# Performance work log

Hardware: AMD Instinct MI355X
Metric: run time of the kernel (lower is better)

## Reference

```python
import jax, jax.numpy as jnp
import numpy as np

N, T, D, H = 128, 64, 1024, 1024
DA = 4  # spatial dim of feature map


def setup_inputs() -> dict:
    key = jax.random.key(0)
    k1, k2, k3, k4, k5 = jax.random.split(key, 5)
    x = jax.random.normal(k1, (N, T, D), dtype=jnp.float32)
    A = jax.random.normal(k2, (N, H, DA, DA), dtype=jnp.float32)
    Wx = jax.random.normal(k3, (D, 4 * H), dtype=jnp.float32) / np.sqrt(D)
    Wh = jax.random.normal(k4, (H, 4 * H), dtype=jnp.float32) / np.sqrt(H)
    Wattn = jax.random.normal(k5, (H, 4 * H), dtype=jnp.float32) / np.sqrt(H)
    b = jnp.zeros((4 * H,), dtype=jnp.float32)
    return {"x": x, "A": A, "Wx": Wx, "Wh": Wh, "Wattn": Wattn, "b": b}


def _dot_product_attention(prev_h, A_flat):
    # prev_h: (N, H), A_flat: (N, H, L) with L = DA*DA
    scores = jnp.einsum('nh,nhl->nl', prev_h, A_flat) / jnp.sqrt(jnp.float32(H))
    w = jax.nn.softmax(scores, axis=-1)              # (N, L)
    attn = jnp.einsum('nhl,nl->nh', A_flat, w)       # (N, H)
    return attn


def reference(x, A, Wx, Wh, Wattn, b):
    A_flat = A.reshape(A.shape[0], A.shape[1], -1)   # (N, H, L)
    h0 = A.mean(axis=(2, 3))                          # (N, H)
    c0 = h0
    x_t = jnp.swapaxes(x, 0, 1)                       # (T, N, D)

    def step(carry, xt):
        h, c = carry
        attn = _dot_product_attention(h, A_flat)
        a = xt @ Wx + h @ Wh + attn @ Wattn + b       # (N, 4H)
        i, f, o, g = jnp.split(a, 4, axis=1)
        i = jax.nn.sigmoid(i)
        f = jax.nn.sigmoid(f)
        o = jax.nn.sigmoid(o)
        g = jnp.tanh(g)
        c_next = f * c + i * g
        h_next = o * jnp.tanh(c_next)
        return (h_next, c_next), h_next

    _, hn = jax.lax.scan(step, (h0, c0), x_t)         # hn: (T, N, H)
    return jnp.swapaxes(hn, 0, 1)                      # (N, T, H)
```

## Files before the change

kernel.cpp:

```cpp
#include <hip/hip_runtime.h>
#include <stdint.h>
#include <math.h>

typedef __attribute__((ext_vector_type(8))) short short8;
typedef __attribute__((ext_vector_type(4))) short short4v;
typedef __attribute__((ext_vector_type(4))) float f32x4;

__device__ __forceinline__ short f2bf(float f){
  union { float f; uint32_t u; } x; x.f = f;
  uint32_t r = x.u + 0x7fffu + ((x.u >> 16) & 1u);
  return (short)(r >> 16);
}
__device__ __forceinline__ float bf2f(short s){
  union { uint32_t u; float f; } x; x.u = ((uint32_t)(uint16_t)s) << 16;
  return x.f;
}

__device__ __forceinline__ unsigned ld_llc_u32(const void* p){
  return __hip_atomic_load((const unsigned*)p, __ATOMIC_RELAXED, __HIP_MEMORY_SCOPE_AGENT);
}
__device__ __forceinline__ void st_llc_u32(void* p, unsigned v){
  __hip_atomic_store((unsigned*)p, v, __ATOMIC_RELAXED, __HIP_MEMORY_SCOPE_AGENT);
}


__global__ __launch_bounds__(256) void k_wt(const float* __restrict__ Wx,
                                            const float* __restrict__ Wh,
                                            const float* __restrict__ Wattn,
                                            short* __restrict__ W3T){
  __shared__ float tile[64][65];
  int bk = blockIdx.x % 48, bj = blockIdx.x / 48;
  int tx = threadIdx.x & 63, ty = threadIdx.x >> 6;
  int k0 = bk * 64, j0 = bj * 64;
  #pragma unroll
  for (int i = 0; i < 16; ++i){
    int kk = ty * 16 + i;
    int k = k0 + kk;
    const float* src = (k < 1024) ? (Wx + (size_t)k * 4096)
                     : (k < 2048) ? (Wh + (size_t)(k - 1024) * 4096)
                                  : (Wattn + (size_t)(k - 2048) * 4096);
    tile[kk][tx] = src[j0 + tx];
  }
  __syncthreads();
  #pragma unroll
  for (int i = 0; i < 16; ++i){
    int jj = ty * 16 + i;
    W3T[(size_t)(j0 + jj) * 3072 + k0 + tx] = f2bf(tile[tx][jj]);
  }
}

__global__ __launch_bounds__(256) void k_cast(const float* __restrict__ in,
                                              short* __restrict__ out, int n4){
  int i = blockIdx.x * 256 + threadIdx.x;
  if (i >= n4) return;
  float4 v = ((const float4*)in)[i];
  short4v o; o[0] = f2bf(v.x); o[1] = f2bf(v.y); o[2] = f2bf(v.z); o[3] = f2bf(v.w);
  *(short4v*)(out + (size_t)i * 4) = o;
}

__global__ __launch_bounds__(256) void k_castA(const float* __restrict__ A,
                                               short* __restrict__ Abf,
                                               short* __restrict__ Atr){
  const int n = blockIdx.x;
  const int tid = threadIdx.x;
  __shared__ short tile[256][17];
  for (int it = 0; it < 4; ++it){
    int h = it * 256 + tid;
    const float* src = A + ((size_t)n * 1024 + h) * 16;
    short o[16];
    #pragma unroll
    for (int l = 0; l < 16; ++l) o[l] = f2bf(src[l]);
    short8 p0, p1;
    #pragma unroll
    for (int l = 0; l < 8; ++l){ p0[l] = o[l]; p1[l] = o[8 + l]; }
    short8* dst = (short8*)(Abf + ((size_t)n * 1024 + h) * 16);
    dst[0] = p0; dst[1] = p1;
    #pragma unroll
    for (int l = 0; l < 16; ++l) tile[tid][l] = o[l];
    __syncthreads();
    {
      int l = tid >> 4, hc = (tid & 15) * 16;
      short tmp[16];
      #pragma unroll
      for (int k = 0; k < 16; ++k) tmp[k] = tile[hc + k][l];
      short8 q0, q1;
      #pragma unroll
      for (int k = 0; k < 8; ++k){ q0[k] = tmp[k]; q1[k] = tmp[8 + k]; }
      short8* d2 = (short8*)(Atr + (size_t)n * 16384 + l * 1024 + it * 256 + hc);
      d2[0] = q0; d2[1] = q1;
    }
    __syncthreads();
  }
}

__global__ __launch_bounds__(256) void k_init(const float* __restrict__ A,
                                              float* __restrict__ c,
                                              short* __restrict__ hb0,
                                              unsigned* __restrict__ flags){
  int idx = blockIdx.x * 256 + threadIdx.x;
  if (idx < 8192) flags[idx] = 0u;
  const float* p = A + (size_t)idx * 16;
  float s = 0.f;
  #pragma unroll
  for (int l = 0; l < 16; ++l) s += p[l];
  s *= (1.f / 16.f);
  c[idx] = s;
  hb0[idx] = f2bf(s);
}

typedef const __attribute__((address_space(1))) uint32_t* gas1_t;
typedef __attribute__((address_space(3))) uint32_t* las3_t;

__global__ __launch_bounds__(256) void k_xwx(const short* __restrict__ xbf,
                                             const short* __restrict__ W3T,
                                             short* __restrict__ xwx){
  __shared__ short ldsA[128 * 64];
  __shared__ short ldsB[128 * 64];
  const int tid  = threadIdx.x;
  const int lane = tid & 63;
  const int wave = tid >> 6;
  const int orig = blockIdx.x;
  const int wg = (orig & 7) * 256 + (orig >> 3);
  const int n_t = wg >> 6;
  const int m_t = wg & 63;
  const int m0 = m_t * 128;
  const int n0 = n_t * 128;
  const int ra = lane & 15;
  const int q  = lane >> 4;

  f32x4 acc[4][4];
  #pragma unroll
  for (int mf = 0; mf < 4; ++mf)
    #pragma unroll
    for (int jf = 0; jf < 4; ++jf) acc[mf][jf] = f32x4{0.f,0.f,0.f,0.f};

  const int wm = wave >> 1;
  const int wn = wave & 1;

  for (int kt = 0; kt < 16; ++kt){
    const int kb = kt * 64;
    #pragma unroll
    for (int r = 0; r < 4; ++r){
      int id = (wave * 4 + r) * 64 + lane;
      int row = id >> 3, c = id & 7;
      int csrc = c ^ (row & 7);
      const short* src = xbf + (size_t)(m0 + row) * 1024 + kb + csrc * 8;
      short* dst = ldsA + (wave * 4 + r) * 512;
      __builtin_amdgcn_global_load_lds((gas1_t)(const void*)src, (las3_t)(void*)dst, 16, 0, 0);
    }
    #pragma unroll
    for (int r = 0; r < 4; ++r){
      int id = (wave * 4 + r) * 64 + lane;
      int row = id >> 3, c = id & 7;
      int csrc = c ^ (row & 7);
      const short* src = W3T + (size_t)(n0 + row) * 3072 + kb + csrc * 8;
      short* dst = ldsB + (wave * 4 + r) * 512;
      __builtin_amdgcn_global_load_lds((gas1_t)(const void*)src, (las3_t)(void*)dst, 16, 0, 0);
    }
    asm volatile("s_waitcnt vmcnt(0)" ::: "memory");
    __syncthreads();

    #pragma unroll
    for (int kk = 0; kk < 64; kk += 32){
      const int cc = (kk >> 3) + q;
      short8 af[4], bfr[4];
      #pragma unroll
      for (int mf = 0; mf < 4; ++mf){
        int row = wm * 64 + mf * 16 + ra;
        af[mf] = *(const short8*)(ldsA + row * 64 + ((cc ^ (row & 7)) << 3));
      }
      #pragma unroll
      for (int jf = 0; jf < 4; ++jf){
        int row = wn * 64 + jf * 16 + ra;
        bfr[jf] = *(const short8*)(ldsB + row * 64 + ((cc ^ (row & 7)) << 3));
      }
      #pragma unroll
      for (int mf = 0; mf < 4; ++mf)
        #pragma unroll
        for (int jf = 0; jf < 4; ++jf)
          acc[mf][jf] = __builtin_amdgcn_mfma_f32_16x16x32_bf16(af[mf], bfr[jf], acc[mf][jf], 0, 0, 0);
    }
    __syncthreads();
  }

  #pragma unroll
  for (int mf = 0; mf < 4; ++mf)
    #pragma unroll
    for (int jf = 0; jf < 4; ++jf)
      #pragma unroll
      for (int i = 0; i < 4; ++i){
        int row = m0 + wm * 64 + mf * 16 + q * 4 + i;
        int col = n0 + wn * 64 + jf * 16 + ra;
        xwx[(size_t)row * 4096 + col] = f2bf(acc[mf][jf][i]);
      }
}

__global__ __launch_bounds__(256) void k_pw(const short* __restrict__ W3T,
                                            const short* __restrict__ Atr,
                                            short* __restrict__ P){
  const int tid  = threadIdx.x;
  const int lane = tid & 63;
  const int wave = tid >> 6;
  const int blk  = blockIdx.x;
  const int n    = blk >> 4;
  const int jblk = blk & 15;
  const int j0   = jblk * 256 + wave * 64;
  const int ra = lane & 15;
  const int q  = lane >> 4;

  f32x4 acc[4];
  #pragma unroll
  for (int mf = 0; mf < 4; ++mf) acc[mf] = f32x4{0.f,0.f,0.f,0.f};

  auto loadA = [&](int ks, int mf) -> short8 {
    return *(const short8*)(W3T + (size_t)(j0 + mf*16 + ra) * 3072 + 2048 + ks * 32 + q * 8);
  };
  auto loadB = [&](int ks) -> short8 {
    return *(const short8*)(Atr + (size_t)n * 16384 + ra * 1024 + ks * 32 + q * 8);
  };

  short8 aC[4], bC, aN[4], bN;
  #pragma unroll
  for (int mf = 0; mf < 4; ++mf) aC[mf] = loadA(0, mf);
  bC = loadB(0);
  for (int ks = 0; ks < 32; ++ks){
    bool more = (ks + 1) < 32;
    if (more){
      #pragma unroll
      for (int mf = 0; mf < 4; ++mf) aN[mf] = loadA(ks + 1, mf);
      bN = loadB(ks + 1);
    }
    #pragma unroll
    for (int mf = 0; mf < 4; ++mf)
      acc[mf] = __builtin_amdgcn_mfma_f32_16x16x32_bf16(aC[mf], bC, acc[mf], 0, 0, 0);
    if (more){
      #pragma unroll
      for (int mf = 0; mf < 4; ++mf) aC[mf] = aN[mf];
      bC = bN;
    }
  }
  #pragma unroll
  for (int mf = 0; mf < 4; ++mf)
    #pragma unroll
    for (int i = 0; i < 4; ++i){
      int j = j0 + mf * 16 + q * 4 + i;
      P[(size_t)(n * 4096 + j) * 16 + ra] = f2bf(acc[mf][i]);
    }
}

__global__ __launch_bounds__(512, 1) void k_loop(
    const short* __restrict__ W3T,
    const short* __restrict__ Abf,
    const short* __restrict__ P,
    short* __restrict__ hbuf,
    float* __restrict__ wbuf,
    const float* __restrict__ cbuf,
    const short* __restrict__ xwx,
    const float* __restrict__ bias,
    float* __restrict__ out,
    unsigned* __restrict__ flags)
{
  __shared__ short Wl[32768];
  __shared__ float redu[4096];
  __shared__ float sred[4][16];
  __shared__ float wlds[64][16];

  unsigned* flagsB = flags;
  unsigned* wtag   = flags + 4096;

  const int tid  = threadIdx.x;
  const int lane = tid & 63;
  const int wave = tid >> 6;
  const int bid  = blockIdx.x;
  const int mh   = bid & 1;
  const int jb   = bid >> 1;
  const int u0   = jb * 8;
  const int ra   = lane & 15;
  const int q    = lane >> 4;
  const int mf2  = wave & 1;
  const int kh   = wave >> 1;
  const bool isScore = (bid < 128);
  const int n_s  = mh * 64 + jb;

  #pragma unroll
  for (int it = 0; it < 8; ++it){
    int c16 = it * 512 + tid;
    int jl = c16 >> 7;
    int kc = c16 & 127;
    int jf = jl >> 4, rr = jl & 15;
    int j = (jf * 2 + (rr >> 3)) * 1024 + u0 + (rr & 7);
    short8 v = *(const short8*)(W3T + (size_t)j * 3072 + 1024 + kc * 8);
    int pc = (jf * 16 + rr) * 128 + (kc ^ (rr & 7));
    *(short8*)(Wl + pc * 8) = v;
  }

  short8 af0[4], af1[4];
  const int hh0 = tid * 4;
  if (wave < 4 && isScore){
    #pragma unroll
    for (int j = 0; j < 4; ++j){
      const short8* ap = (const short8*)(Abf + ((size_t)n_s * 1024 + hh0 + j) * 16);
      af0[j] = ap[0]; af1[j] = ap[1];
    }
  }

  const int n_loc = tid >> 3, uu = tid & 7;
  const int cn = mh * 64 + n_loc;
  const int cu = u0 + uu;
  float creg = cbuf[(size_t)cn * 1024 + cu];
  const float b0 = bias[cu], b1 = bias[1024 + cu], b2 = bias[2048 + cu], b3 = bias[3072 + cu];
  __syncthreads();

  for (int t = 0; t < 64; ++t){
    const short* hRp = hbuf + (size_t)t * 131072;
    short*       hWp = hbuf + (size_t)(t + 1) * 131072;
    float*       wT  = wbuf + (size_t)t * 4096;

    if (t > 0){
      const unsigned tgt = (unsigned)t;
      for (;;){
        unsigned v0 = ld_llc_u32(&flagsB[(mh * 128 + lane * 2)     * 16]);
        unsigned v1 = ld_llc_u32(&flagsB[(mh * 128 + lane * 2 + 1) * 16]);
        unsigned mn = v0 < v1 ? v0 : v1;
        if (__all(mn >= tgt)) break;
        __builtin_amdgcn_s_sleep(1);
      }
    }

    if (wave < 4 && isScore){
      uint64_t hq = *(const uint64_t*)(hRp + n_s * 1024 + hh0);
      float hv[4];
      #pragma unroll
      for (int j = 0; j < 4; ++j) hv[j] = bf2f((short)((hq >> (16 * j)) & 0xffffu));
      float sc[16];
      #pragma unroll
      for (int l = 0; l < 8; ++l){
        float s0 = 0.f, s1 = 0.f;
        #pragma unroll
        for (int j = 0; j < 4; ++j){ s0 += hv[j] * bf2f(af0[j][l]); s1 += hv[j] * bf2f(af1[j][l]); }
        sc[l] = s0; sc[8 + l] = s1;
      }
      #pragma unroll
      for (int off = 1; off < 64; off <<= 1)
        #pragma unroll
        for (int l = 0; l < 16; ++l) sc[l] += __shfl_xor(sc[l], off);
      if (lane == 0)
        #pragma unroll
        for (int l = 0; l < 16; ++l) sred[wave][l] = sc[l];
    }
    __syncthreads();

    if (wave == 0 && isScore){
      float s[16], mx = -1e30f, sum = 0.f;
      #pragma unroll
      for (int l = 0; l < 16; ++l){
        s[l] = (sred[0][l] + sred[1][l] + sred[2][l] + sred[3][l]) * 0.03125f;
        mx = fmaxf(mx, s[l]);
      }
      #pragma unroll
      for (int l = 0; l < 16; ++l){ s[l] = __expf(s[l] - mx); sum += s[l]; }
      const float inv = 1.f / sum;
      #pragma unroll
      for (int l = 0; l < 16; ++l){
        if (lane == l){
          union { float f; unsigned u; } cv; cv.f = s[l] * inv;
          st_llc_u32(&wT[n_s * 32 + l], cv.u);
        }
      }
      asm volatile("s_waitcnt vmcnt(0)" ::: "memory");
      if (lane == 0) st_llc_u32(&wtag[n_s * 16], (unsigned)(t + 1));
    }

    const short* xp = xwx + ((size_t)cn * 64 + t) * 4096;
    const short xw0 = xp[cu], xw1 = xp[1024 + cu], xw2 = xp[2048 + cu], xw3 = xp[3072 + cu];

    auto loadA = [&](int ks, int m) -> short8 {
      const int kk = kh * 256 + ks * 32 + q * 8;
      const int row = mh * 64 + mf2 * 32 + m * 16 + ra;
      return *(const short8*)(hRp + row * 1024 + kk);
    };
    auto loadB = [&](int ks, int jf) -> short8 {
      const int kcg = kh * 32 + ks * 4 + q;
      const int sw = kcg ^ (ra & 7);
      return *(const short8*)(Wl + (((jf * 16 + ra) * 128) + sw) * 8);
    };

    short8 Ab[4][2], Bb[2][2];
    Bb[0][0] = loadB(0, 0); Bb[0][1] = loadB(0, 1);
    Bb[1][0] = loadB(1, 0); Bb[1][1] = loadB(1, 1);
    #pragma unroll
    for (int p = 0; p < 4; ++p){ Ab[p][0] = loadA(p, 0); Ab[p][1] = loadA(p, 1); }

    f32x4 acc[2][2];
    acc[0][0] = f32x4{0.f,0.f,0.f,0.f}; acc[0][1] = f32x4{0.f,0.f,0.f,0.f};
    acc[1][0] = f32x4{0.f,0.f,0.f,0.f}; acc[1][1] = f32x4{0.f,0.f,0.f,0.f};

    #pragma unroll
    for (int ks = 0; ks < 8; ++ks){
      short8 av0 = Ab[ks & 3][0], av1 = Ab[ks & 3][1];
      short8 bv0 = Bb[ks & 1][0], bv1 = Bb[ks & 1][1];
      if (ks < 4){ Ab[ks & 3][0] = loadA(ks + 4, 0); Ab[ks & 3][1] = loadA(ks + 4, 1); }
      if (ks < 6){ Bb[ks & 1][0] = loadB(ks + 2, 0); Bb[ks & 1][1] = loadB(ks + 2, 1); }
      acc[0][0] = __builtin_amdgcn_mfma_f32_16x16x32_bf16(av0, bv0, acc[0][0], 0, 0, 0);
      acc[0][1] = __builtin_amdgcn_mfma_f32_16x16x32_bf16(av0, bv1, acc[0][1], 0, 0, 0);
      acc[1][0] = __builtin_amdgcn_mfma_f32_16x16x32_bf16(av1, bv0, acc[1][0], 0, 0, 0);
      acc[1][1] = __builtin_amdgcn_mfma_f32_16x16x32_bf16(av1, bv1, acc[1][1], 0, 0, 0);
    }

    auto ridx = [&](int m2, int khq, int m, int jf) -> float* {
      return &redu[((((m2 * 2 + khq) * 2 + m) * 2 + jf) * 64 + lane) * 4];
    };
    if (kh & 1){
      *(f32x4*)ridx(mf2, kh >> 1, 0, 0) = acc[0][0];
      *(f32x4*)ridx(mf2, kh >> 1, 0, 1) = acc[0][1];
      *(f32x4*)ridx(mf2, kh >> 1, 1, 0) = acc[1][0];
      *(f32x4*)ridx(mf2, kh >> 1, 1, 1) = acc[1][1];
    }
    __syncthreads();
    if (!(kh & 1)){
      acc[0][0] += *(const f32x4*)ridx(mf2, kh >> 1, 0, 0);
      acc[0][1] += *(const f32x4*)ridx(mf2, kh >> 1, 0, 1);
      acc[1][0] += *(const f32x4*)ridx(mf2, kh >> 1, 1, 0);
      acc[1][1] += *(const f32x4*)ridx(mf2, kh >> 1, 1, 1);
    }
    if (wave == 2){
      const unsigned tgt = (unsigned)(t + 1);
      for (;;){
        unsigned v = ld_llc_u32(&wtag[(mh * 64 + lane) * 16]);
        if (__all(v >= tgt)) break;
        __builtin_amdgcn_s_sleep(1);
      }
      const f32x4* wp = (const f32x4*)(wT + (mh * 64 + lane) * 32);
      f32x4 w0 = wp[0], w1 = wp[1], w2 = wp[2], w3 = wp[3];
      f32x4* wd = (f32x4*)&wlds[lane][0];
      wd[0] = w0; wd[1] = w1; wd[2] = w2; wd[3] = w3;
    }
    __syncthreads();
    if (kh == 2){
      *(f32x4*)ridx(mf2, 0, 0, 0) = acc[0][0];
      *(f32x4*)ridx(mf2, 0, 0, 1) = acc[0][1];
      *(f32x4*)ridx(mf2, 0, 1, 0) = acc[1][0];
      *(f32x4*)ridx(mf2, 0, 1, 1) = acc[1][1];
    }
    __syncthreads();
    if (kh == 0){
      acc[0][0] += *(const f32x4*)ridx(mf2, 0, 0, 0);
      acc[0][1] += *(const f32x4*)ridx(mf2, 0, 0, 1);
      acc[1][0] += *(const f32x4*)ridx(mf2, 0, 1, 0);
      acc[1][1] += *(const f32x4*)ridx(mf2, 0, 1, 1);
    }
    __syncthreads();
    if (kh == 0){
      #pragma unroll
      for (int m = 0; m < 2; ++m)
        #pragma unroll
        for (int jf = 0; jf < 2; ++jf){
          const int g = jf * 2 + (ra >> 3);
          const int nl = mf2 * 32 + m * 16 + q * 4;
          #pragma unroll
          for (int i = 0; i < 4; ++i)
            redu[g * 512 + (nl + i) * 8 + (ra & 7)] = acc[m][jf][i];
        }
    }
    __syncthreads();

    float hn;
    {
      float wl[16];
      #pragma unroll
      for (int l = 0; l < 16; ++l) wl[l] = wlds[n_loc][l];
      float pg[4];
      #pragma unroll
      for (int g = 0; g < 4; ++g){
        const short8* pp = (const short8*)(P + ((size_t)cn * 4096 + g * 1024 + cu) * 16);
        short8 pa = pp[0], pb = pp[1];
        float s = 0.f;
        #pragma unroll
        for (int l = 0; l < 8; ++l){ s += bf2f(pa[l]) * wl[l]; s += bf2f(pb[l]) * wl[8 + l]; }
        pg[g] = s;
      }
      const float av = redu[tid]        + bf2f(xw0) + pg[0] + b0;
      const float fv = redu[512 + tid]  + bf2f(xw1) + pg[1] + b1;
      const float ov = redu[1024 + tid] + bf2f(xw2) + pg[2] + b2;
      const float gv = redu[1536 + tid] + bf2f(xw3) + pg[3] + b3;
      const float ig = 1.f / (1.f + __expf(-av));
      const float fg = 1.f / (1.f + __expf(-fv));
      const float og = 1.f / (1.f + __expf(-ov));
      const float gcl = fminf(fmaxf(gv, -20.f), 20.f);
      const float e2g = __expf(2.f * gcl);
      const float gg = (e2g - 1.f) / (e2g + 1.f);
      creg = fg * creg + ig * gg;
      const float ccl = fminf(fmaxf(creg, -20.f), 20.f);
      const float e2c = __expf(2.f * ccl);
      const float th = (e2c - 1.f) / (e2c + 1.f);
      hn = og * th;
      const float hn2 = __shfl_xor(hn, 1);
      if ((tid & 1) == 0){
        unsigned pk = (unsigned)(unsigned short)f2bf(hn)
                    | ((unsigned)(unsigned short)f2bf(hn2) << 16);
        st_llc_u32(hWp + (size_t)cn * 1024 + cu, pk);
      }
    }
    asm volatile("s_waitcnt vmcnt(0)" ::: "memory");
    __syncthreads();
    if (tid == 0 && t < 63) st_llc_u32(&flagsB[(mh * 128 + jb) * 16], (unsigned)(t + 1));
    __builtin_nontemporal_store(hn, &out[((size_t)cn * 64 + t) * 1024 + cu]);
  }
}


extern "C" void kernel_launch(void* const* d_in, const int* in_sizes, int n_in,
                              void* d_out, int out_size, void* d_ws, size_t ws_size,
                              hipStream_t stream)
{
  const float* x     = (const float*)d_in[0];
  const float* A     = (const float*)d_in[1];
  const float* Wx    = (const float*)d_in[2];
  const float* Wh    = (const float*)d_in[3];
  const float* Wattn = (const float*)d_in[4];
  const float* b     = (const float*)d_in[5];
  float* out = (float*)d_out;
  char* ws = (char*)d_ws;

  short*    W3T   = (short*)(ws + 0);
  short*    Abf   = (short*)(ws + 25165824);
  short*    Atr   = (short*)(ws + 29360128);
  short*    xbf   = (short*)(ws + 33554432);
  short*    xwx   = (short*)(ws + 50331648);
  short*    P     = (short*)(ws + 117440512);
  short*    hbuf  = (short*)(ws + 134217728);
  float*    wbuf  = (float*)(ws + 151257088);
  float*    cbuf  = (float*)(ws + 152305664);
  unsigned* flags = (unsigned*)(ws + 152829952);

  hipLaunchKernelGGL(k_wt,    dim3(48 * 64), dim3(256), 0, stream, Wx, Wh, Wattn, W3T);
  hipLaunchKernelGGL(k_cast,  dim3(2097152 / 256), dim3(256), 0, stream, x, xbf, 2097152);
  hipLaunchKernelGGL(k_castA, dim3(128), dim3(256), 0, stream, A, Abf, Atr);
  hipLaunchKernelGGL(k_init,  dim3(512), dim3(256), 0, stream, A, cbuf, hbuf, flags);
  hipLaunchKernelGGL(k_xwx,   dim3(2048), dim3(256), 0, stream, xbf, W3T, xwx);
  hipLaunchKernelGGL(k_pw,    dim3(2048), dim3(256), 0, stream, W3T, Atr, P);
  hipLaunchKernelGGL(k_loop,  dim3(256), dim3(512), 0, stream,
                     W3T, Abf, P, hbuf, wbuf, cbuf, xwx, b, out, flags);
}
```

Baseline: 892.8 us.

## Rebalance recurrent GEMM K-split and replace barrier tree with flag-synced reduction

Moves the attention-score computation to waves 4-7 and has them combine partial scores through LDS flags instead of a block barrier. In score blocks the K range is split unevenly so those waves get less of the GEMM, and the two-level reduction with four barriers becomes a single partial-sum buffer summed by waves 0-1. The x-projection load is hoisted ahead of the flag wait. This aims to cut per-timestep barrier count and load imbalance on the serial critical path, at the cost of more LDS and spin-waiting on workgroup-scope flags.

```diff
diff --git a/kernel.cpp b/kernel.cpp
--- a/kernel.cpp
+++ b/kernel.cpp
@@ -248,6 +248,40 @@
     }
 }
 
+template<int ITERS>
+__device__ __forceinline__ void gemm_slice(const short* __restrict__ hRp,
+                                           const short* __restrict__ Wl_,
+                                           int kbase, int mh, int mf2,
+                                           int ra, int q, f32x4 acc[2][2]){
+  const int kb8 = kbase >> 3;
+  auto loadA = [&](int ks, int m) -> short8 {
+    const int k = kbase + ks * 32 + q * 8;
+    const int row = mh * 64 + mf2 * 32 + m * 16 + ra;
+    return *(const short8*)(hRp + row * 1024 + k);
+  };
+  auto loadB = [&](int ks, int jf) -> short8 {
+    const int kcg = kb8 + ks * 4 + q;
+    const int sw = kcg ^ (ra & 7);
+    return *(const short8*)(Wl_ + (((jf * 16 + ra) * 128) + sw) * 8);
+  };
+  short8 Ab[4][2], Bb[2][2];
+  Bb[0][0] = loadB(0, 0); Bb[0][1] = loadB(0, 1);
+  Bb[1][0] = loadB(1, 0); Bb[1][1] = loadB(1, 1);
+  #pragma unroll
+  for (int p = 0; p < 4; ++p){ Ab[p][0] = loadA(p, 0); Ab[p][1] = loadA(p, 1); }
+  #pragma unroll
+  for (int ks = 0; ks < ITERS; ++ks){
+    short8 av0 = Ab[ks & 3][0], av1 = Ab[ks & 3][1];
+    short8 bv0 = Bb[ks & 1][0], bv1 = Bb[ks & 1][1];
+    if (ks + 4 < ITERS){ Ab[ks & 3][0] = loadA(ks + 4, 0); Ab[ks & 3][1] = loadA(ks + 4, 1); }
+    if (ks + 2 < ITERS){ Bb[ks & 1][0] = loadB(ks + 2, 0); Bb[ks & 1][1] = loadB(ks + 2, 1); }
+    acc[0][0] = __builtin_amdgcn_mfma_f32_16x16x32_bf16(av0, bv0, acc[0][0], 0, 0, 0);
+    acc[0][1] = __builtin_amdgcn_mfma_f32_16x16x32_bf16(av0, bv1, acc[0][1], 0, 0, 0);
+    acc[1][0] = __builtin_amdgcn_mfma_f32_16x16x32_bf16(av1, bv0, acc[1][0], 0, 0, 0);
+    acc[1][1] = __builtin_amdgcn_mfma_f32_16x16x32_bf16(av1, bv1, acc[1][1], 0, 0, 0);
+  }
+}
+
 __global__ __launch_bounds__(512, 1) void k_loop(
     const short* __restrict__ W3T,
     const short* __restrict__ Abf,
@@ -261,9 +295,11 @@
     unsigned* __restrict__ flags)
 {
   __shared__ short Wl[32768];
-  __shared__ float redu[4096];
-  __shared__ float sred[4][16];
+  __shared__ float part[6][1024];
+  __shared__ float fin[2048];
+  __shared__ float sred[3][16];
   __shared__ float wlds[64][16];
+  __shared__ unsigned lflag[3];
 
   unsigned* flagsB = flags;
   unsigned* wtag   = flags + 4096;
@@ -293,10 +329,12 @@
     int pc = (jf * 16 + rr) * 128 + (kc ^ (rr & 7));
     *(short8*)(Wl + pc * 8) = v;
   }
+  if (tid < 3) lflag[tid] = 0u;
 
   short8 af0[4], af1[4];
-  const int hh0 = tid * 4;
-  if (wave < 4 && isScore){
+  const int st_ = tid - 256;
+  const int hh0 = st_ * 4;
+  if (wave >= 4 && isScore){
     #pragma unroll
     for (int j = 0; j < 4; ++j){
       const short8* ap = (const short8*)(Abf + ((size_t)n_s * 1024 + hh0 + j) * 16);
@@ -315,6 +353,9 @@
     const short* hRp = hbuf + (size_t)t * 131072;
     short*       hWp = hbuf + (size_t)(t + 1) * 131072;
     float*       wT  = wbuf + (size_t)t * 4096;
+
+    const short* xp = xwx + ((size_t)cn * 64 + t) * 4096;
+    const short xw0 = xp[cu], xw1 = xp[1024 + cu], xw2 = xp[2048 + cu], xw3 = xp[3072 + cu];
 
     if (t > 0){
       const unsigned tgt = (unsigned)t;
@@ -327,7 +368,7 @@
       }
     }
 
-    if (wave < 4 && isScore){
+    if (isScore && wave >= 4){
       uint64_t hq = *(const uint64_t*)(hRp + n_s * 1024 + hh0);
       float hv[4];
       #pragma unroll
@@ -344,123 +385,97 @@
       for (int off = 1; off < 64; off <<= 1)
         #pragma unroll
         for (int l = 0; l < 16; ++l) sc[l] += __shfl_xor(sc[l], off);
-      if (lane == 0)
-        #pragma unroll
-        for (int l = 0; l < 16; ++l) sred[wave][l] = sc[l];
-    }
-    __syncthreads();
-
-    if (wave == 0 && isScore){
-      float s[16], mx = -1e30f, sum = 0.f;
-      #pragma unroll
-      for (int l = 0; l < 16; ++l){
-        s[l] = (sred[0][l] + sred[1][l] + sred[2][l] + sred[3][l]) * 0.03125f;
-        mx = fmaxf(mx, s[l]);
-      }
-      #pragma unroll
-      for (int l = 0; l < 16; ++l){ s[l] = __expf(s[l] - mx); sum += s[l]; }
-      const float inv = 1.f / sum;
-      #pragma unroll
-      for (int l = 0; l < 16; ++l){
-        if (lane == l){
-          union { float f; unsigned u; } cv; cv.f = s[l] * inv;
-          st_llc_u32(&wT[n_s * 32 + l], cv.u);
+      if (wave > 4){
+        if (lane == 0){
+          #pragma unroll
+          for (int l = 0; l < 16; ++l) sred[wave - 5][l] = sc[l];
+          __hip_atomic_store(&lflag[wave - 5], (unsigned)(t + 1),
+                             __ATOMIC_RELEASE, __HIP_MEMORY_SCOPE_WORKGROUP);
         }
-      }
-      asm volatile("s_waitcnt vmcnt(0)" ::: "memory");
-      if (lane == 0) st_llc_u32(&wtag[n_s * 16], (unsigned)(t + 1));
-    }
-
-    const short* xp = xwx + ((size_t)cn * 64 + t) * 4096;
-    const short xw0 = xp[cu], xw1 = xp[1024 + cu], xw2 = xp[2048 + cu], xw3 = xp[3072 + cu];
-
-    auto loadA = [&](int ks, int m) -> short8 {
-      const int kk = kh * 256 + ks * 32 + q * 8;
-      const int row = mh * 64 + mf2 * 32 + m * 16 + ra;
-      return *(const short8*)(hRp + row * 1024 + kk);
-    };
-    auto loadB = [&](int ks, int jf) -> short8 {
-      const int kcg = kh * 32 + ks * 4 + q;
-      const int sw = kcg ^ (ra & 7);
-      return *(const short8*)(Wl + (((jf * 16 + ra) * 128) + sw) * 8);
-    };
-
-    short8 Ab[4][2], Bb[2][2];
-    Bb[0][0] = loadB(0, 0); Bb[0][1] = loadB(0, 1);
-    Bb[1][0] = loadB(1, 0); Bb[1][1] = loadB(1, 1);
-    #pragma unroll
-    for (int p = 0; p < 4; ++p){ Ab[p][0] = loadA(p, 0); Ab[p][1] = loadA(p, 1); }
+      } else {
+        const unsigned tgt = (unsigned)(t + 1);
+        for (;;){
+          unsigned a = __hip_atomic_load(&lflag[0], __ATOMIC_ACQUIRE, __HIP_MEMORY_SCOPE_WORKGROUP);
+          unsigned b = __hip_atomic_load(&lflag[1], __ATOMIC_ACQUIRE, __HIP_MEMORY_SCOPE_WORKGROUP);
+          unsigned c = __hip_atomic_load(&lflag[2], __ATOMIC_ACQUIRE, __HIP_MEMORY_SCOPE_WORKGROUP);
+          unsigned mn = a < b ? a : b; mn = c < mn ? c : mn;
+          if (mn >= tgt) break;
+          __builtin_amdgcn_s_sleep(1);
+        }
+        float s[16], mx = -1e30f, sum = 0.f;
+        #pragma unroll
+        for (int l = 0; l < 16; ++l){
+          s[l] = (sc[l] + sred[0][l] + sred[1][l] + sred[2][l]) * 0.03125f;
+          mx = fmaxf(mx, s[l]);
+        }
+        #pragma unroll
+        for (int l = 0; l < 16; ++l){ s[l] = __expf(s[l] - mx); sum += s[l]; }
+        const float inv = 1.f / sum;
+        #pragma unroll
+        for (int l = 0; l < 16; ++l){
+          if (lane == l){
+            union { float f; unsigned u; } cv; cv.f = s[l] * inv;
+            st_llc_u32(&wT[n_s * 32 + l], cv.u);
+          }
+        }
+        asm volatile("s_waitcnt vmcnt(0)" ::: "memory");
+        if (lane == 0) st_llc_u32(&wtag[n_s * 16], (unsigned)(t + 1));
+      }
+    }
 
     f32x4 acc[2][2];
     acc[0][0] = f32x4{0.f,0.f,0.f,0.f}; acc[0][1] = f32x4{0.f,0.f,0.f,0.f};
     acc[1][0] = f32x4{0.f,0.f,0.f,0.f}; acc[1][1] = f32x4{0.f,0.f,0.f,0.f};
-
-    #pragma unroll
-    for (int ks = 0; ks < 8; ++ks){
-      short8 av0 = Ab[ks & 3][0], av1 = Ab[ks & 3][1];
-      short8 bv0 = Bb[ks & 1][0], bv1 = Bb[ks & 1][1];
-      if (ks < 4){ Ab[ks & 3][0] = loadA(ks + 4, 0); Ab[ks & 3][1] = loadA(ks + 4, 1); }
-      if (ks < 6){ Bb[ks & 1][0] = loadB(ks + 2, 0); Bb[ks & 1][1] = loadB(ks + 2, 1); }
-      acc[0][0] = __builtin_amdgcn_mfma_f32_16x16x32_bf16(av0, bv0, acc[0][0], 0, 0, 0);
-      acc[0][1] = __builtin_amdgcn_mfma_f32_16x16x32_bf16(av0, bv1, acc[0][1], 0, 0, 0);
-      acc[1][0] = __builtin_amdgcn_mfma_f32_16x16x32_bf16(av1, bv0, acc[1][0], 0, 0, 0);
-      acc[1][1] = __builtin_amdgcn_mfma_f32_16x16x32_bf16(av1, bv1, acc[1][1], 0, 0, 0);
-    }
-
-    auto ridx = [&](int m2, int khq, int m, int jf) -> float* {
-      return &redu[((((m2 * 2 + khq) * 2 + m) * 2 + jf) * 64 + lane) * 4];
-    };
-    if (kh & 1){
-      *(f32x4*)ridx(mf2, kh >> 1, 0, 0) = acc[0][0];
-      *(f32x4*)ridx(mf2, kh >> 1, 0, 1) = acc[0][1];
-      *(f32x4*)ridx(mf2, kh >> 1, 1, 0) = acc[1][0];
-      *(f32x4*)ridx(mf2, kh >> 1, 1, 1) = acc[1][1];
-    }
-    __syncthreads();
-    if (!(kh & 1)){
-      acc[0][0] += *(const f32x4*)ridx(mf2, kh >> 1, 0, 0);
-      acc[0][1] += *(const f32x4*)ridx(mf2, kh >> 1, 0, 1);
-      acc[1][0] += *(const f32x4*)ridx(mf2, kh >> 1, 1, 0);
-      acc[1][1] += *(const f32x4*)ridx(mf2, kh >> 1, 1, 1);
-    }
-    if (wave == 2){
+    if (isScore){
+      if      (kh == 0) gemm_slice<10>(hRp, Wl, 0,   mh, mf2, ra, q, acc);
+      else if (kh == 1) gemm_slice<10>(hRp, Wl, 320, mh, mf2, ra, q, acc);
+      else if (kh == 2) gemm_slice<6> (hRp, Wl, 640, mh, mf2, ra, q, acc);
+      else              gemm_slice<6> (hRp, Wl, 832, mh, mf2, ra, q, acc);
+    } else {
+      if      (kh == 0) gemm_slice<8>(hRp, Wl, 0,   mh, mf2, ra, q, acc);
+      else if (kh == 1) gemm_slice<8>(hRp, Wl, 256, mh, mf2, ra, q, acc);
+      else if (kh == 2) gemm_slice<8>(hRp, Wl, 512, mh, mf2, ra, q, acc);
+      else              gemm_slice<8>(hRp, Wl, 768, mh, mf2, ra, q, acc);
+    }
+
+    if (wave >= 2){
+      const int pidx = wave - 2;
+      #pragma unroll
+      for (int m = 0; m < 2; ++m)
+        #pragma unroll
+        for (int jf = 0; jf < 2; ++jf)
+          *(f32x4*)&part[pidx][((m * 2 + jf) * 64 + lane) * 4] = acc[m][jf];
+    }
+    __syncthreads();
+
+    if (wave < 2){
+      #pragma unroll
+      for (int m = 0; m < 2; ++m)
+        #pragma unroll
+        for (int jf = 0; jf < 2; ++jf){
+          const int x = ((m * 2 + jf) * 64 + lane) * 4;
+          f32x4 s = acc[m][jf];
+          s += *(const f32x4*)&part[0 + mf2][x];
+          s += *(const f32x4*)&part[2 + mf2][x];
+          s += *(const f32x4*)&part[4 + mf2][x];
+          const int g = jf * 2 + (ra >> 3);
+          const int nl = mf2 * 32 + m * 16 + q * 4;
+          #pragma unroll
+          for (int i = 0; i < 4; ++i)
+            fin[g * 512 + (nl + i) * 8 + (ra & 7)] = s[i];
+        }
+    }
+    if (wave == 6){
       const unsigned tgt = (unsigned)(t + 1);
       for (;;){
         unsigned v = ld_llc_u32(&wtag[(mh * 64 + lane) * 16]);
         if (__all(v >= tgt)) break;
         __builtin_amdgcn_s_sleep(1);
       }
-      const f32x4* wp = (const f32x4*)(wT + (mh * 64 + lane) * 32);
+      const f32x4* wp = (const f32x4*)(wbuf + (size_t)t * 4096 + (mh * 64 + lane) * 32);
       f32x4 w0 = wp[0], w1 = wp[1], w2 = wp[2], w3 = wp[3];
       f32x4* wd = (f32x4*)&wlds[lane][0];
       wd[0] = w0; wd[1] = w1; wd[2] = w2; wd[3] = w3;
-    }
-    __syncthreads();
-    if (kh == 2){
-      *(f32x4*)ridx(mf2, 0, 0, 0) = acc[0][0];
-      *(f32x4*)ridx(mf2, 0, 0, 1) = acc[0][1];
-      *(f32x4*)ridx(mf2, 0, 1, 0) = acc[1][0];
-      *(f32x4*)ridx(mf2, 0, 1, 1) = acc[1][1];
-    }
-    __syncthreads();
-    if (kh == 0){
-      acc[0][0] += *(const f32x4*)ridx(mf2, 0, 0, 0);
-      acc[0][1] += *(const f32x4*)ridx(mf2, 0, 0, 1);
-      acc[1][0] += *(const f32x4*)ridx(mf2, 0, 1, 0);
-      acc[1][1] += *(const f32x4*)ridx(mf2, 0, 1, 1);
-    }
-    __syncthreads();
-    if (kh == 0){
-      #pragma unroll
-      for (int m = 0; m < 2; ++m)
-        #pragma unroll
-        for (int jf = 0; jf < 2; ++jf){
-          const int g = jf * 2 + (ra >> 3);
-          const int nl = mf2 * 32 + m * 16 + q * 4;
-          #pragma unroll
-          for (int i = 0; i < 4; ++i)
-            redu[g * 512 + (nl + i) * 8 + (ra & 7)] = acc[m][jf][i];
-        }
     }
     __syncthreads();
 
@@ -479,10 +494,10 @@
         for (int l = 0; l < 8; ++l){ s += bf2f(pa[l]) * wl[l]; s += bf2f(pb[l]) * wl[8 + l]; }
         pg[g] = s;
       }
-      const float av = redu[tid]        + bf2f(xw0) + pg[0] + b0;
-      const float fv = redu[512 + tid]  + bf2f(xw1) + pg[1] + b1;
-      const float ov = redu[1024 + tid] + bf2f(xw2) + pg[2] + b2;
-      const float gv = redu[1536 + tid] + bf2f(xw3) + pg[3] + b3;
+      const float av = fin[tid]        + bf2f(xw0) + pg[0] + b0;
+      const float fv = fin[512 + tid]  + bf2f(xw1) + pg[1] + b1;
+      const float ov = fin[1024 + tid] + bf2f(xw2) + pg[2] + b2;
+      const float gv = fin[1536 + tid] + bf2f(xw3) + pg[3] + b3;
       const float ig = 1.f / (1.f + __expf(-av));
       const float fg = 1.f / (1.f + __expf(-fv));
       const float og = 1.f / (1.f + __expf(-ov));
```

Result: slower. 918.1 us (+2.8%).
